# Kernel optimization log

Hardware: AMD Instinct MI355X
Metric: run time of the kernel (lower is better)

The kernel has to match this reference:

```python
import jax, jax.numpy as jnp
import numpy as np

N = 100000      # nodes
E = 1600000     # edges
NSG2 = 20000    # subgraph2 count
NSG = 2000      # subgraph count
NG = 64         # graphs
D = 64          # hidden dim
L = 5           # conv layers


def setup_inputs() -> dict:
    key = jax.random.key(0)
    ks = jax.random.split(key, 40)
    f = lambda i, shape: (jax.random.normal(ks[i], shape, jnp.float32) * 0.05)
    inp = {
        'z': jax.random.randint(ks[0], (N, 2), 0, 100),
        'edge_index': jax.random.randint(ks[1], (2, E), 0, N),
        'node_to_subgraph2': jax.random.randint(ks[2], (N,), 0, NSG2),
        'subgraph2_to_subgraph': jax.random.randint(ks[3], (NSG2,), 0, NSG),
        'subgraph_to_graph': jax.random.randint(ks[4], (NSG,), 0, NG),
        # learned params (stacked across the 5 layers where identical shape)
        'z_emb': f(5, (L, 100, D)),
        'trans_W': f(6, (L - 1, 2 * D, D)),  # transform_before_conv, layers 1..4
        'trans_b': f(7, (L - 1, D)),
        'conv_W': f(8, (L, D, D)),           # GatedGraphConv weight (num_layers=1)
        'gru_Wih': f(9, (L, D, 3 * D)),
        'gru_bih': f(10, (L, 3 * D)),
        'gru_Whh': f(11, (L, D, 3 * D)),
        'gru_bhh': f(12, (L, 3 * D)),
        'ep_W1': f(13, (D, D)), 'ep_b1': f(14, (D,)),
        'ep_W2': f(15, (D, D)), 'ep_b2': f(16, (D,)),
        'np_W1': f(17, (D, D)), 'np_b1': f(18, (D,)),
        'np_W2': f(19, (D, D)), 'np_b2': f(20, (D,)),
        'fc1_W': f(21, (D, 32)), 'fc1_b': f(22, (32,)),
        'fc2_W': f(23, (32, 16)), 'fc2_b': f(24, (16,)),
        'fc3_W': f(25, (16, 1)), 'fc3_b': f(26, (1,)),
    }
    return inp


def _gated_conv(x, src, dst, W, Wih, bih, Whh, bhh):
    # GatedGraphConv(out=64, num_layers=1): m = aggr_add(x_j @ W), x = GRUCell(m, x)
    h = x @ W                                            # [N, D]
    m = jax.ops.segment_sum(h[src], dst, num_segments=N)  # scatter-add messages
    gi = m @ Wih + bih                                   # [N, 3D]
    gh = x @ Whh + bhh
    ir, iz, inn = jnp.split(gi, 3, axis=-1)
    hr, hz, hn = jnp.split(gh, 3, axis=-1)
    r = jax.nn.sigmoid(ir + hr)
    zg = jax.nn.sigmoid(iz + hz)
    n = jnp.tanh(inn + r * hn)
    return (1.0 - zg) * n + zg * x


def reference(z, edge_index, node_to_subgraph2, subgraph2_to_subgraph, subgraph_to_graph,
              z_emb, trans_W, trans_b, conv_W, gru_Wih, gru_bih, gru_Whh, gru_bhh,
              ep_W1, ep_b1, ep_W2, ep_b2, np_W1, np_b1, np_W2, np_b2,
              fc1_W, fc1_b, fc2_W, fc2_b, fc3_W, fc3_b):
    src, dst = edge_index[0], edge_index[1]
    x = None
    for layer in range(L):
        ze = z_emb[layer][z].sum(axis=1)  # [N,2,D] -> [N,D]
        if x is None:
            x = ze
        else:
            x = jnp.concatenate([x, ze], axis=-1) @ trans_W[layer - 1] + trans_b[layer - 1]
        x = _gated_conv(x, src, dst, conv_W[layer], gru_Wih[layer], gru_bih[layer],
                        gru_Whh[layer], gru_bhh[layer])
    # 3-level add pooling with MLPs in between
    x = jax.ops.segment_sum(x, node_to_subgraph2, num_segments=NSG2)
    x = jax.nn.relu(x @ ep_W1 + ep_b1) @ ep_W2 + ep_b2
    x = jax.ops.segment_sum(x, subgraph2_to_subgraph, num_segments=NSG)
    x = jax.nn.relu(x @ np_W1 + np_b1) @ np_W2 + np_b2
    x = jax.ops.segment_sum(x, subgraph_to_graph, num_segments=NG)
    x = jax.nn.elu(x @ fc1_W + fc1_b)
    x = jax.nn.elu(x @ fc2_W + fc2_b)
    return x @ fc3_W + fc3_b  # [NG, 1]
```

## Files before the change

kernel.cpp:

```cpp
#include <hip/hip_runtime.h>
#include <hip/hip_bf16.h>

constexpr int N    = 100000;
constexpr int E    = 1600000;
constexpr int NSG2 = 20000;
constexpr int NSG  = 2000;
constexpr int NG   = 64;
constexpr int D    = 64;
constexpr int L    = 5;

constexpr int CB    = (N + 255) / 256;
constexpr int NSTR  = 8;
constexpr int SCAP2 = 768;

typedef __attribute__((ext_vector_type(8))) short short8v;
typedef __attribute__((ext_vector_type(4))) float f32x4;

__device__ __forceinline__ float sigm(float x) { return 1.0f / (1.0f + expf(-x)); }
__device__ __forceinline__ float elu(float x)  { return x > 0.0f ? x : (expf(x) - 1.0f); }

__device__ __forceinline__ unsigned short f2b(float f) {
    union { float f; unsigned u; } x; x.f = f;
    unsigned r = (x.u + 0x7FFFu + ((x.u >> 16) & 1u)) >> 16;
    return (unsigned short)r;
}
__device__ __forceinline__ float b2f(unsigned short h) {
    union { unsigned u; float f; } x; x.u = (unsigned)h << 16;
    return x.f;
}

__global__ __launch_bounds__(256) void prep_kernel(const float* __restrict__ convW,
                                                   const float* __restrict__ Wih,
                                                   float* __restrict__ WihP) {
    int idx = blockIdx.x * 256 + threadIdx.x;
    if (idx >= L * 64 * 192) return;
    int l = idx / (64 * 192);
    int rem = idx % (64 * 192);
    int i = rem / 192, j = rem % 192;
    const float* W  = convW + l * 64 * 64;
    const float* Wi = Wih  + l * 64 * 192;
    float acc = 0.0f;
    for (int t = 0; t < 64; ++t) acc = fmaf(W[i * 64 + t], Wi[t * 192 + j], acc);
    WihP[idx] = acc;
}

__global__ __launch_bounds__(256) void packg_kernel(const float* __restrict__ WihP,
                                                    const float* __restrict__ gWhh,
                                                    unsigned short* __restrict__ Wgpk) {
    int idx = blockIdx.x * 256 + threadIdx.x;
    if (idx >= L * 2 * 12 * 2 * 64) return;
    int lane = idx & 63;
    int r1 = idx >> 6;
    int t  = r1 & 1;
    int r2 = r1 >> 1;
    int nt = r2 % 12;
    int lm = r2 / 12;
    int mat = lm & 1, l = lm >> 1;
    const float* W = mat ? (gWhh + (size_t)l * 64 * 192) : (WihP + (size_t)l * 64 * 192);
    int n  = nt * 16 + (lane & 15);
    int k0 = t * 32 + (lane >> 4) * 8;
    short8v v;
#pragma unroll
    for (int j = 0; j < 8; ++j) v[j] = (short)f2b(W[(k0 + j) * 192 + n]);
    *(short8v*)(Wgpk + (size_t)idx * 8) = v;
}

__global__ __launch_bounds__(256) void packt_kernel(const float* __restrict__ tW,
                                                    unsigned short* __restrict__ tWpk) {
    int idx = blockIdx.x * 256 + threadIdx.x;
    if (idx >= (L - 1) * 4 * 4 * 64) return;
    int lane = idx & 63;
    int r1 = idx >> 6;
    int t  = r1 & 3;
    int r2 = r1 >> 2;
    int nt = r2 & 3;
    int lm = r2 >> 2;
    const float* W = tW + (size_t)lm * 128 * 64;
    int n  = nt * 16 + (lane & 15);
    int k0 = t * 32 + (lane >> 4) * 8;
    short8v v;
#pragma unroll
    for (int j = 0; j < 8; ++j) v[j] = (short)f2b(W[(k0 + j) * 64 + n]);
    *(short8v*)(tWpk + (size_t)idx * 8) = v;
}

__global__ void csrA_kernel(const int* __restrict__ src, const int* __restrict__ dst,
                            int* __restrict__ bcnt, unsigned* __restrict__ tmp) {
    int stripe = blockIdx.x & (NSTR - 1);
    for (int e = blockIdx.x * blockDim.x + threadIdx.x; e < E; e += gridDim.x * blockDim.x) {
        int d = dst[e];
        int cell = stripe * CB + (d >> 8);
        int pos = atomicAdd(&bcnt[cell * 16], 1);
        if (pos < SCAP2)
            tmp[(size_t)cell * SCAP2 + pos] = ((unsigned)(d & 255) << 17) | (unsigned)src[e];
    }
}

__global__ __launch_bounds__(256) void csrB_kernel(const unsigned* __restrict__ tmp,
                                                   const int* __restrict__ bcnt,
                                                   int* __restrict__ rowptr,
                                                   int* __restrict__ col) {
    __shared__ int hist[256];
    __shared__ int scanb[256];
    __shared__ int cur[256];
    __shared__ int scnt[NSTR];
    __shared__ int red[4];
    int b = blockIdx.x, t = threadIdx.x;
    int lane = t & 63, wid = t >> 6;

    int myb = 0;
    for (int cb = t; cb < b; cb += 256) {
        int tot = 0;
#pragma unroll
        for (int s = 0; s < NSTR; ++s) tot += min(bcnt[(s * CB + cb) * 16], SCAP2);
        myb += tot;
    }
#pragma unroll
    for (int off = 32; off > 0; off >>= 1) myb += __shfl_down(myb, off, 64);
    if (lane == 0) red[wid] = myb;
    if (t < NSTR) scnt[t] = min(bcnt[(t * CB + b) * 16], SCAP2);
    hist[t] = 0;
    __syncthreads();
    int base = red[0] + red[1] + red[2] + red[3];

    for (int s = 0; s < NSTR; ++s)
        for (int i = t; i < scnt[s]; i += 256)
            atomicAdd(&hist[tmp[((size_t)s * CB + b) * SCAP2 + i] >> 17], 1);
    __syncthreads();

    scanb[t] = hist[t];
    __syncthreads();
    for (int off = 1; off < 256; off <<= 1) {
        int v = (t >= off) ? scanb[t - off] : 0;
        __syncthreads();
        scanb[t] += v;
        __syncthreads();
    }
    int excl = scanb[t] - hist[t];
    int node = b * 256 + t;
    if (node < N) rowptr[node] = base + excl;
    if (b == CB - 1 && t == 255) rowptr[N] = base + scanb[255];
    cur[t] = base + excl;
    __syncthreads();

    for (int s = 0; s < NSTR; ++s)
        for (int i = t; i < scnt[s]; i += 256) {
            unsigned rec = tmp[((size_t)s * CB + b) * SCAP2 + i];
            int pos = atomicAdd(&cur[rec >> 17], 1);
            col[pos] = (int)(rec & 0x1FFFFu);
        }
}

__global__ __launch_bounds__(256) void embed_kernel(const int* __restrict__ z,
                                                    const float* __restrict__ zemb0,
                                                    unsigned short* __restrict__ xb) {
    int idx = blockIdx.x * 256 + threadIdx.x;
    if (idx >= N * 16) return;
    int n = idx >> 4, k4 = idx & 15;
    float4 e0 = ((const float4*)(zemb0 + (size_t)z[n * 2] * 64))[k4];
    float4 e1 = ((const float4*)(zemb0 + (size_t)z[n * 2 + 1] * 64))[k4];
    ushort4 b; b.x = f2b(e0.x + e1.x); b.y = f2b(e0.y + e1.y);
    b.z = f2b(e0.z + e1.z); b.w = f2b(e0.w + e1.w);
    ((ushort4*)xb)[idx] = b;
}

template<int HAS_T>
__global__ __launch_bounds__(256) void fused_kernel(const unsigned short* __restrict__ xb_in,
                                                    unsigned short* __restrict__ xb_out,
                                                    const int* __restrict__ rowptr,
                                                    const int* __restrict__ col,
                                                    const unsigned short* __restrict__ Wgpk_l,
                                                    const float* __restrict__ bih,
                                                    const float* __restrict__ bhh,
                                                    const int* __restrict__ z,
                                                    const float* __restrict__ zemb_next,
                                                    const unsigned short* __restrict__ tWpk_next,
                                                    const float* __restrict__ tb_next,
                                                    const int* __restrict__ n2s2,
                                                    float* __restrict__ sg2) {
    __shared__ union {
        struct { unsigned short s[32][72]; unsigned short x[32][72]; } p1;
        unsigned short a[32][136];
    } u;
    int tid = threadIdx.x;
    int node0 = blockIdx.x * 32;
    int lane = tid & 63, w = tid >> 6;

    {
        int g8 = lane >> 3, cj = lane & 7;
        int nl = w * 8 + g8;
        int node = node0 + nl;
        float4 ownx = ((const float4*)(xb_in + (size_t)node * 64))[cj];
        int beg = rowptr[node], end = rowptr[node + 1];
        float a[8] = {};
        const unsigned short* __restrict__ xbc = xb_in + cj * 8;
        int i = beg;
        for (; i + 8 <= end; i += 8) {
            int u0 = col[i],     u1 = col[i + 1], u2 = col[i + 2], u3 = col[i + 3];
            int u4 = col[i + 4], u5 = col[i + 5], u6 = col[i + 6], u7 = col[i + 7];
            short8v v0 = *(const short8v*)(xbc + (size_t)u0 * 64);
            short8v v1 = *(const short8v*)(xbc + (size_t)u1 * 64);
            short8v v2 = *(const short8v*)(xbc + (size_t)u2 * 64);
            short8v v3 = *(const short8v*)(xbc + (size_t)u3 * 64);
            short8v v4 = *(const short8v*)(xbc + (size_t)u4 * 64);
            short8v v5 = *(const short8v*)(xbc + (size_t)u5 * 64);
            short8v v6 = *(const short8v*)(xbc + (size_t)u6 * 64);
            short8v v7 = *(const short8v*)(xbc + (size_t)u7 * 64);
#pragma unroll
            for (int j = 0; j < 8; ++j)
                a[j] += ((b2f((unsigned short)v0[j]) + b2f((unsigned short)v1[j])) +
                         (b2f((unsigned short)v2[j]) + b2f((unsigned short)v3[j]))) +
                        ((b2f((unsigned short)v4[j]) + b2f((unsigned short)v5[j])) +
                         (b2f((unsigned short)v6[j]) + b2f((unsigned short)v7[j])));
        }
        for (; i + 4 <= end; i += 4) {
            int u0 = col[i], u1 = col[i + 1], u2 = col[i + 2], u3 = col[i + 3];
            short8v v0 = *(const short8v*)(xbc + (size_t)u0 * 64);
            short8v v1 = *(const short8v*)(xbc + (size_t)u1 * 64);
            short8v v2 = *(const short8v*)(xbc + (size_t)u2 * 64);
            short8v v3 = *(const short8v*)(xbc + (size_t)u3 * 64);
#pragma unroll
            for (int j = 0; j < 8; ++j)
                a[j] += (b2f((unsigned short)v0[j]) + b2f((unsigned short)v1[j])) +
                        (b2f((unsigned short)v2[j]) + b2f((unsigned short)v3[j]));
        }
        for (; i + 2 <= end; i += 2) {
            int u0 = col[i], u1 = col[i + 1];
            short8v v0 = *(const short8v*)(xbc + (size_t)u0 * 64);
            short8v v1 = *(const short8v*)(xbc + (size_t)u1 * 64);
#pragma unroll
            for (int j = 0; j < 8; ++j)
                a[j] += b2f((unsigned short)v0[j]) + b2f((unsigned short)v1[j]);
        }
        if (i < end) {
            short8v v = *(const short8v*)(xbc + (size_t)col[i] * 64);
#pragma unroll
            for (int j = 0; j < 8; ++j) a[j] += b2f((unsigned short)v[j]);
        }
        short8v r;
#pragma unroll
        for (int j = 0; j < 8; ++j) r[j] = (short)f2b(a[j]);
        *(short8v*)&u.p1.s[nl][cj * 8] = r;
        *(float4*)&u.p1.x[nl][cj * 8] = ownx;
    }
    __syncthreads();

    int lr = lane & 15, lg = lane >> 4;
    int ch = w * 16 + lr;
    short8v as_[2][2], ax_[2][2];
#pragma unroll
    for (int mt = 0; mt < 2; ++mt)
#pragma unroll
        for (int t = 0; t < 2; ++t) {
            int row = mt * 16 + lr, koff = t * 32 + lg * 8;
            as_[mt][t] = *(const short8v*)&u.p1.s[row][koff];
            ax_[mt][t] = *(const short8v*)&u.p1.x[row][koff];
        }
    float xres[2][4];
#pragma unroll
    for (int mt = 0; mt < 2; ++mt)
#pragma unroll
        for (int reg = 0; reg < 4; ++reg)
            xres[mt][reg] = b2f(u.p1.x[mt * 16 + lg * 4 + reg][ch]);
    if (HAS_T) __syncthreads();

    f32x4 accA[3][2] = {};
    f32x4 accB[3][2] = {};
#pragma unroll
    for (int g = 0; g < 3; ++g) {
        int nt = g * 4 + w;
#pragma unroll
        for (int t = 0; t < 2; ++t) {
            const unsigned short* pA = Wgpk_l + ((size_t)((0 * 12 + nt) * 2 + t) * 64 + lane) * 8;
            const unsigned short* pB = Wgpk_l + ((size_t)((1 * 12 + nt) * 2 + t) * 64 + lane) * 8;
            short8v bA = *(const short8v*)pA;
            short8v bB = *(const short8v*)pB;
#pragma unroll
            for (int mt = 0; mt < 2; ++mt) {
                accA[g][mt] = __builtin_amdgcn_mfma_f32_16x16x32_bf16(as_[mt][t], bA, accA[g][mt], 0, 0, 0);
                accB[g][mt] = __builtin_amdgcn_mfma_f32_16x16x32_bf16(ax_[mt][t], bB, accB[g][mt], 0, 0, 0);
            }
        }
    }

    float bi0 = bih[ch], bi1 = bih[64 + ch], bi2 = bih[128 + ch];
    float bh0 = bhh[ch], bh1 = bhh[64 + ch], bh2 = bhh[128 + ch];
    float xo[2][4];
#pragma unroll
    for (int mt = 0; mt < 2; ++mt) {
#pragma unroll
        for (int reg = 0; reg < 4; ++reg) {
            float r  = sigm(accA[0][mt][reg] + bi0 + accB[0][mt][reg] + bh0);
            float zg = sigm(accA[1][mt][reg] + bi1 + accB[1][mt][reg] + bh1);
            float nn = tanhf(accA[2][mt][reg] + bi2 + r * (accB[2][mt][reg] + bh2));
            xo[mt][reg] = (1.0f - zg) * nn + zg * xres[mt][reg];
        }
    }

    if (HAS_T == 0) {
#pragma unroll
        for (int mt = 0; mt < 2; ++mt)
#pragma unroll
            for (int reg = 0; reg < 4; ++reg) {
                int m = mt * 16 + lg * 4 + reg;
                atomicAdd(&sg2[(size_t)n2s2[node0 + m] * 64 + ch], xo[mt][reg]);
            }
        return;
    }

#pragma unroll
    for (int mt = 0; mt < 2; ++mt)
#pragma unroll
        for (int reg = 0; reg < 4; ++reg) {
            int m = mt * 16 + lg * 4 + reg;
            u.a[m][ch] = f2b(xo[mt][reg]);
        }
#pragma unroll
    for (int it = 0; it < 2; ++it) {
        int idx = it * 256 + tid;
        int n = idx >> 4, k4 = idx & 15;
        int z0 = z[(node0 + n) * 2], z1 = z[(node0 + n) * 2 + 1];
        float4 e0 = ((const float4*)(zemb_next + (size_t)z0 * 64))[k4];
        float4 e1 = ((const float4*)(zemb_next + (size_t)z1 * 64))[k4];
        ushort4 b;
        b.x = f2b(e0.x + e1.x); b.y = f2b(e0.y + e1.y);
        b.z = f2b(e0.z + e1.z); b.w = f2b(e0.w + e1.w);
        *(ushort4*)&u.a[n][64 + k4 * 4] = b;
    }
    __syncthreads();

    f32x4 tacc[2] = {};
#pragma unroll
    for (int t = 0; t < 4; ++t) {
        const unsigned short* pB = tWpk_next + ((size_t)(w * 4 + t) * 64 + lane) * 8;
        short8v bf = *(const short8v*)pB;
#pragma unroll
        for (int mt = 0; mt < 2; ++mt) {
            int row = mt * 16 + lr, koff = t * 32 + lg * 8;
            short8v af = *(const short8v*)&u.a[row][koff];
            tacc[mt] = __builtin_amdgcn_mfma_f32_16x16x32_bf16(af, bf, tacc[mt], 0, 0, 0);
        }
    }
    float tbc = tb_next[ch];

    __shared__ unsigned short outb[32][72];
#pragma unroll
    for (int mt = 0; mt < 2; ++mt)
#pragma unroll
        for (int reg = 0; reg < 4; ++reg) {
            int m = mt * 16 + lg * 4 + reg;
            outb[m][ch] = f2b(tacc[mt][reg] + tbc);
        }
    __syncthreads();
    {
        int r = tid >> 3, q = tid & 7;
        *(float4*)(xb_out + (size_t)(node0 + r) * 64 + q * 8) = *(const float4*)&outb[r][q * 8];
    }
}

__global__ void pool_kernel(const float* __restrict__ in, const int* __restrict__ idx,
                            float* __restrict__ out, int rows) {
    int i = blockIdx.x * 256 + threadIdx.x;
    if (i >= rows * 64) return;
    int r = i >> 6, c = i & 63;
    atomicAdd(out + (size_t)idx[r] * 64 + c, in[i]);
}

__global__ __launch_bounds__(256) void mlp_kernel(float* __restrict__ buf,
                                                  const float* __restrict__ W1,
                                                  const float* __restrict__ b1,
                                                  const float* __restrict__ W2,
                                                  const float* __restrict__ b2) {
    __shared__ float in_t[4][64];
    __shared__ float h_t[4][64];
    int tid = threadIdx.x;
    int c = tid & 63, r = tid >> 6;
    int row0 = blockIdx.x * 4;
    in_t[r][c] = buf[(size_t)(row0 + r) * 64 + c];
    __syncthreads();
    float acc = b1[c];
    for (int k = 0; k < 64; ++k) acc = fmaf(in_t[r][k], W1[k * 64 + c], acc);
    h_t[r][c] = fmaxf(acc, 0.0f);
    __syncthreads();
    acc = b2[c];
    for (int k = 0; k < 64; ++k) acc = fmaf(h_t[r][k], W2[k * 64 + c], acc);
    buf[(size_t)(row0 + r) * 64 + c] = acc;
}

__global__ __launch_bounds__(256) void final_kernel(const float* __restrict__ g,
                                                    const float* __restrict__ fc1W, const float* __restrict__ fc1b,
                                                    const float* __restrict__ fc2W, const float* __restrict__ fc2b,
                                                    const float* __restrict__ fc3W, const float* __restrict__ fc3b,
                                                    float* __restrict__ out) {
    __shared__ float gt[64][64];
    __shared__ float h1[64][32];
    __shared__ float h2[64][16];
    int tid = threadIdx.x;
    for (int i = tid; i < 64 * 64; i += 256) gt[i >> 6][i & 63] = g[i];
    __syncthreads();
    for (int i = tid; i < 64 * 32; i += 256) {
        int r = i >> 5, c = i & 31;
        float acc = fc1b[c];
        for (int k = 0; k < 64; ++k) acc = fmaf(gt[r][k], fc1W[k * 32 + c], acc);
        h1[r][c] = elu(acc);
    }
    __syncthreads();
    for (int i = tid; i < 64 * 16; i += 256) {
        int r = i >> 4, c = i & 15;
        float acc = fc2b[c];
        for (int k = 0; k < 32; ++k) acc = fmaf(h1[r][k], fc2W[k * 16 + c], acc);
        h2[r][c] = elu(acc);
    }
    __syncthreads();
    if (tid < 64) {
        float acc = fc3b[0];
        for (int k = 0; k < 16; ++k) acc = fmaf(h2[tid][k], fc3W[k], acc);
        out[tid] = acc;
    }
}

extern "C" void kernel_launch(void* const* d_in, const int* in_sizes, int n_in,
                              void* d_out, int out_size, void* d_ws, size_t ws_size,
                              hipStream_t stream) {
    const int*   z     = (const int*)d_in[0];
    const int*   ei    = (const int*)d_in[1];
    const int*   n2s2  = (const int*)d_in[2];
    const int*   s22s  = (const int*)d_in[3];
    const int*   s2g   = (const int*)d_in[4];
    const float* z_emb = (const float*)d_in[5];
    const float* tW    = (const float*)d_in[6];
    const float* tb    = (const float*)d_in[7];
    const float* convW = (const float*)d_in[8];
    const float* gWih  = (const float*)d_in[9];
    const float* gbih  = (const float*)d_in[10];
    const float* gWhh  = (const float*)d_in[11];
    const float* gbhh  = (const float*)d_in[12];
    const float* epW1  = (const float*)d_in[13];
    const float* epb1  = (const float*)d_in[14];
    const float* epW2  = (const float*)d_in[15];
    const float* epb2  = (const float*)d_in[16];
    const float* npW1  = (const float*)d_in[17];
    const float* npb1  = (const float*)d_in[18];
    const float* npW2  = (const float*)d_in[19];
    const float* npb2  = (const float*)d_in[20];
    const float* fc1W  = (const float*)d_in[21];
    const float* fc1b  = (const float*)d_in[22];
    const float* fc2W  = (const float*)d_in[23];
    const float* fc2b  = (const float*)d_in[24];
    const float* fc3W  = (const float*)d_in[25];
    const float* fc3b  = (const float*)d_in[26];

    const int* srcp = ei;
    const int* dstp = ei + E;

    unsigned short* xbA = (unsigned short*)d_ws;
    unsigned short* xbB = xbA + (size_t)N * D;
    float*          WihP = (float*)(xbB + (size_t)N * D);
    int*            rowptr = (int*)(WihP + L * 64 * 192);
    int*            colbuf = rowptr + (N + 1);
    uintptr_t pal = (uintptr_t)(colbuf + E);
    pal = (pal + 15) & ~(uintptr_t)15;
    unsigned short* Wgpk = (unsigned short*)pal;
    unsigned short* tWpk = Wgpk + (size_t)L * 2 * 12 * 2 * 64 * 8;
    uintptr_t pal2 = (uintptr_t)(tWpk + (size_t)(L - 1) * 4 * 4 * 64 * 8);
    pal2 = (pal2 + 15) & ~(uintptr_t)15;
    unsigned* tmp  = (unsigned*)pal2;
    int*      bcnt = (int*)(tmp + (size_t)CB * NSTR * SCAP2);
    float*    sg2  = (float*)(bcnt + (size_t)CB * NSTR * 16);
    float*    sg   = sg2 + (size_t)NSG2 * D;
    float*    gbuf = sg + (size_t)NSG * D;

    hipMemsetAsync(bcnt, 0, (size_t)CB * NSTR * 16 * sizeof(int), stream);
    hipMemsetAsync(sg2, 0, (size_t)(NSG2 + NSG + NG) * D * sizeof(float), stream);

    prep_kernel<<<(L * 64 * 192 + 255) / 256, 256, 0, stream>>>(convW, gWih, WihP);
    packg_kernel<<<(L * 2 * 12 * 2 * 64 + 255) / 256, 256, 0, stream>>>(WihP, gWhh, Wgpk);
    packt_kernel<<<((L - 1) * 4 * 4 * 64 + 255) / 256, 256, 0, stream>>>(tW, tWpk);

    csrA_kernel<<<4096, 256, 0, stream>>>(srcp, dstp, bcnt, tmp);
    csrB_kernel<<<CB, 256, 0, stream>>>(tmp, bcnt, rowptr, colbuf);

    embed_kernel<<<(N * 16 + 255) / 256, 256, 0, stream>>>(z, z_emb, xbA);

    for (int l = 0; l < L; ++l) {
        const unsigned short* xin = (l & 1) ? xbB : xbA;
        unsigned short*       xout = (l & 1) ? xbA : xbB;
        if (l < L - 1) {
            fused_kernel<1><<<N / 32, 256, 0, stream>>>(
                xin, xout, rowptr, colbuf,
                Wgpk + (size_t)l * 2 * 12 * 2 * 64 * 8,
                gbih + (size_t)l * 192, gbhh + (size_t)l * 192,
                z, z_emb + (size_t)(l + 1) * 100 * 64,
                tWpk + (size_t)l * 4 * 4 * 64 * 8, tb + (size_t)l * 64,
                nullptr, nullptr);
        } else {
            fused_kernel<0><<<N / 32, 256, 0, stream>>>(
                xin, nullptr, rowptr, colbuf,
                Wgpk + (size_t)l * 2 * 12 * 2 * 64 * 8,
                gbih + (size_t)l * 192, gbhh + (size_t)l * 192,
                z, z_emb, tWpk, tb,
                n2s2, sg2);
        }
    }

    mlp_kernel<<<NSG2 / 4, 256, 0, stream>>>(sg2, epW1, epb1, epW2, epb2);
    pool_kernel<<<(NSG2 * D + 255) / 256, 256, 0, stream>>>(sg2, s22s, sg, NSG2);
    mlp_kernel<<<NSG / 4, 256, 0, stream>>>(sg, npW1, npb1, npW2, npb2);
    pool_kernel<<<(NSG * D + 255) / 256, 256, 0, stream>>>(sg, s2g, gbuf, NSG);
    final_kernel<<<1, 256, 0, stream>>>(gbuf, fc1W, fc1b, fc2W, fc2b, fc3W, fc3b, (float*)d_out);
}
```

Measured before the change: 466.2 us.

## Sort nodes by in-degree so each fused-kernel block handles similar-degree nodes

Adds a counting sort of nodes by in-degree (per-block histogram, a scan, and a scatter into a permutation) and makes each fused-kernel block process 32 nodes taken from that permutation instead of 32 consecutive nodes. The aim is to balance the gather loop across the waves of a block and across blocks, reducing divergence and tail imbalance from uneven degrees. In exchange it adds three small preprocessing kernels, an extra indirection for node ids, and scattered rather than contiguous writes and reads of node rows, which loses locality.

```diff
diff --git a/kernel.cpp b/kernel.cpp
--- a/kernel.cpp
+++ b/kernel.cpp
@@ -12,6 +12,7 @@
 constexpr int CB    = (N + 255) / 256;
 constexpr int NSTR  = 8;
 constexpr int SCAP2 = 768;
+constexpr int NBIN  = 48;
 
 typedef __attribute__((ext_vector_type(8))) short short8v;
 typedef __attribute__((ext_vector_type(4))) float f32x4;
@@ -151,6 +152,60 @@
         }
 }
 
+__global__ __launch_bounds__(256) void degh_kernel(const int* __restrict__ rowptr,
+                                                   int* __restrict__ bh) {
+    __shared__ int h[NBIN];
+    int b = blockIdx.x, t = threadIdx.x;
+    if (t < NBIN) h[t] = 0;
+    __syncthreads();
+    int node = b * 256 + t;
+    if (node < N) {
+        int d = rowptr[node + 1] - rowptr[node];
+        atomicAdd(&h[min(d, NBIN - 1)], 1);
+    }
+    __syncthreads();
+    if (t < NBIN) bh[b * NBIN + t] = h[t];
+}
+
+__global__ __launch_bounds__(64) void degscan_kernel(int* __restrict__ bh) {
+    __shared__ int gbase[NBIN + 1];
+    int t = threadIdx.x;
+    if (t < NBIN) {
+        int run = 0;
+        for (int b = 0; b < CB; ++b) {
+            int v = bh[b * NBIN + t];
+            bh[b * NBIN + t] = run;
+            run += v;
+        }
+        gbase[t + 1] = run;
+    }
+    __syncthreads();
+    if (t == 0) {
+        gbase[0] = 0;
+        for (int j = 1; j <= NBIN; ++j) gbase[j] += gbase[j - 1];
+    }
+    __syncthreads();
+    if (t < NBIN) {
+        int g = gbase[t];
+        for (int b = 0; b < CB; ++b) bh[b * NBIN + t] += g;
+    }
+}
+
+__global__ __launch_bounds__(256) void degscat_kernel(const int* __restrict__ rowptr,
+                                                      const int* __restrict__ bh,
+                                                      int* __restrict__ perm) {
+    __shared__ int cur[NBIN];
+    int b = blockIdx.x, t = threadIdx.x;
+    if (t < NBIN) cur[t] = bh[b * NBIN + t];
+    __syncthreads();
+    int node = b * 256 + t;
+    if (node < N) {
+        int d = rowptr[node + 1] - rowptr[node];
+        int pos = atomicAdd(&cur[min(d, NBIN - 1)], 1);
+        perm[pos] = node;
+    }
+}
+
 __global__ __launch_bounds__(256) void embed_kernel(const int* __restrict__ z,
                                                     const float* __restrict__ zemb0,
                                                     unsigned short* __restrict__ xb) {
@@ -169,6 +224,7 @@
                                                     unsigned short* __restrict__ xb_out,
                                                     const int* __restrict__ rowptr,
                                                     const int* __restrict__ col,
+                                                    const int* __restrict__ perm,
                                                     const unsigned short* __restrict__ Wgpk_l,
                                                     const float* __restrict__ bih,
                                                     const float* __restrict__ bhh,
@@ -182,14 +238,18 @@
         struct { unsigned short s[32][72]; unsigned short x[32][72]; } p1;
         unsigned short a[32][136];
     } u;
+    __shared__ int pnodes[32];
     int tid = threadIdx.x;
     int node0 = blockIdx.x * 32;
     int lane = tid & 63, w = tid >> 6;
 
+    if (tid < 32) pnodes[tid] = perm[node0 + tid];
+    __syncthreads();
+
     {
         int g8 = lane >> 3, cj = lane & 7;
         int nl = w * 8 + g8;
-        int node = node0 + nl;
+        int node = pnodes[nl];
         float4 ownx = ((const float4*)(xb_in + (size_t)node * 64))[cj];
         int beg = rowptr[node], end = rowptr[node + 1];
         float a[8] = {};
@@ -303,7 +363,7 @@
 #pragma unroll
             for (int reg = 0; reg < 4; ++reg) {
                 int m = mt * 16 + lg * 4 + reg;
-                atomicAdd(&sg2[(size_t)n2s2[node0 + m] * 64 + ch], xo[mt][reg]);
+                atomicAdd(&sg2[(size_t)n2s2[pnodes[m]] * 64 + ch], xo[mt][reg]);
             }
         return;
     }
@@ -319,7 +379,8 @@
     for (int it = 0; it < 2; ++it) {
         int idx = it * 256 + tid;
         int n = idx >> 4, k4 = idx & 15;
-        int z0 = z[(node0 + n) * 2], z1 = z[(node0 + n) * 2 + 1];
+        int pn = pnodes[n];
+        int z0 = z[pn * 2], z1 = z[pn * 2 + 1];
         float4 e0 = ((const float4*)(zemb_next + (size_t)z0 * 64))[k4];
         float4 e1 = ((const float4*)(zemb_next + (size_t)z1 * 64))[k4];
         ushort4 b;
@@ -354,7 +415,7 @@
     __syncthreads();
     {
         int r = tid >> 3, q = tid & 7;
-        *(float4*)(xb_out + (size_t)(node0 + r) * 64 + q * 8) = *(const float4*)&outb[r][q * 8];
+        *(float4*)(xb_out + (size_t)pnodes[r] * 64 + q * 8) = *(const float4*)&outb[r][q * 8];
     }
 }
 
@@ -466,7 +527,9 @@
     pal2 = (pal2 + 15) & ~(uintptr_t)15;
     unsigned* tmp  = (unsigned*)pal2;
     int*      bcnt = (int*)(tmp + (size_t)CB * NSTR * SCAP2);
-    float*    sg2  = (float*)(bcnt + (size_t)CB * NSTR * 16);
+    int*      perm = bcnt + (size_t)CB * NSTR * 16;
+    int*      bh   = perm + N;
+    float*    sg2  = (float*)(bh + (size_t)CB * NBIN);
     float*    sg   = sg2 + (size_t)NSG2 * D;
     float*    gbuf = sg + (size_t)NSG * D;
 
@@ -479,6 +542,10 @@
 
     csrA_kernel<<<4096, 256, 0, stream>>>(srcp, dstp, bcnt, tmp);
     csrB_kernel<<<CB, 256, 0, stream>>>(tmp, bcnt, rowptr, colbuf);
+
+    degh_kernel<<<CB, 256, 0, stream>>>(rowptr, bh);
+    degscan_kernel<<<1, 64, 0, stream>>>(bh);
+    degscat_kernel<<<CB, 256, 0, stream>>>(rowptr, bh, perm);
 
     embed_kernel<<<(N * 16 + 255) / 256, 256, 0, stream>>>(z, z_emb, xbA);
 
@@ -487,7 +554,7 @@
         unsigned short*       xout = (l & 1) ? xbA : xbB;
         if (l < L - 1) {
             fused_kernel<1><<<N / 32, 256, 0, stream>>>(
-                xin, xout, rowptr, colbuf,
+                xin, xout, rowptr, colbuf, perm,
                 Wgpk + (size_t)l * 2 * 12 * 2 * 64 * 8,
                 gbih + (size_t)l * 192, gbhh + (size_t)l * 192,
                 z, z_emb + (size_t)(l + 1) * 100 * 64,
@@ -495,7 +562,7 @@
                 nullptr, nullptr);
         } else {
             fused_kernel<0><<<N / 32, 256, 0, stream>>>(
-                xin, nullptr, rowptr, colbuf,
+                xin, nullptr, rowptr, colbuf, perm,
                 Wgpk + (size_t)l * 2 * 12 * 2 * 64 * 8,
                 gbih + (size_t)l * 192, gbhh + (size_t)l * 192,
                 z, z_emb, tWpk, tb,
```

Result: slower. 501.5 us (+7.6%).
